# Optimization experiments

Hardware: AMD Instinct MI355X
Metric: run time of the kernel (lower is better)

The kernel has to match this reference:

```python
import jax, jax.numpy as jnp
import numpy as np
from jax import lax

# Module constants (from init_kwargs)
K = 1.0            # conductivity
H = 1.0 / 1023.0   # grid spacing
VALUE = 0.0        # Dirichlet boundary value
STENCIL = np.array([[0.0, 0.25, 0.0],
                    [0.25, 0.0, 0.25],
                    [0.0, 0.25, 0.0]], dtype=np.float32)


def setup_inputs() -> dict:
    key = jax.random.key(0)
    k1, k2 = jax.random.split(key)
    B, C, Hn, Wn = 16, 1, 1024, 1024
    u = jax.random.normal(k1, (B, C, Hn, Wn), dtype=jnp.float32)
    f = jax.random.normal(k2, (B, C, Hn, Wn), dtype=jnp.float32)
    # conv weight: (out=1, in=1, 3, 3), repeated over in_channels (=1 here)
    weight = jnp.asarray(STENCIL).reshape(1, 1, 3, 3)
    return {"u": u, "f": f, "weight": weight}


def reference(u, f, weight):
    # v = detached interior of u, padded with the Dirichlet value
    v_int = lax.stop_gradient(u[..., 1:-1, 1:-1])           # [B,1,H-2,W-2]
    v = jnp.pad(v_int, ((0, 0), (0, 0), (1, 1), (1, 1)),
                mode="constant", constant_values=VALUE)      # [B,1,H,W]
    # 5-point Jacobi stencil, VALID conv -> interior shape [B,1,H-2,W-2]
    conv = lax.conv_general_dilated(
        v, weight, window_strides=(1, 1), padding="VALID",
        dimension_numbers=("NCHW", "OIHW", "NCHW"))
    cof = -(H ** 2) / (K * 4.0)
    source = lax.stop_gradient((cof * f)[..., 1:-1, 1:-1])
    # interior <- stencil(v) + source; boundary stays at Dirichlet VALUE
    out = v.at[..., 1:-1, 1:-1].set(conv + source)
    return out
```

## Files before the change

### kernel.cpp

```cpp
#include <hip/hip_runtime.h>

#define IMG_W 1024
#define IMG_H 1024
#define RPB   4

__global__ __launch_bounds__(256) void dir_rhs_kernel(
    const float* __restrict__ u,
    const float* __restrict__ f,
    const float* __restrict__ wt,
    float* __restrict__ out)
{
    __shared__ float2 halo[RPB + 2][256];

    const int tid = threadIdx.x;
    const int j0  = tid << 2;
    const int gb  = blockIdx.x;
    const int b   = gb >> 8;
    const int r0  = (gb & 255) << 2;
    const size_t img = (size_t)b << 20;

    const float w00 = wt[0], w01 = wt[1], w02 = wt[2];
    const float w10 = wt[3], w11 = wt[4], w12 = wt[5];
    const float w20 = wt[6], w21 = wt[7], w22 = wt[8];
    const float cof = (float)(-(1.0 / 1023.0) * (1.0 / 1023.0) / 4.0);

    float4 stage[RPB + 2];
    #pragma unroll
    for (int k = 0; k < RPB + 2; k++) {
        const int grow = r0 - 1 + k;
        if (grow >= 1 && grow <= IMG_H - 2) {
            stage[k] = *(const float4*)(u + img + (size_t)grow * IMG_W + j0);
        } else {
            stage[k] = make_float4(0.f, 0.f, 0.f, 0.f);
        }
    }
    float4 fr[RPB];
    #pragma unroll
    for (int k = 0; k < RPB; k++) {
        fr[k] = *(const float4*)(f + img + (size_t)(r0 + k) * IMG_W + j0);
    }
    #pragma unroll
    for (int k = 0; k < RPB + 2; k++) {
        if (tid == 0)   stage[k].x = 0.f;
        if (tid == 255) stage[k].w = 0.f;
        halo[k][tid] = make_float2(stage[k].x, stage[k].w);
    }
    __syncthreads();

    const int tl = (tid == 0)   ? 0   : tid - 1;
    const int tr = (tid == 255) ? 255 : tid + 1;

    #pragma unroll
    for (int k = 0; k < RPB; k++) {
        const int grow = r0 + k;
        float4* o4 = (float4*)(out + img + (size_t)grow * IMG_W + j0);
        if (grow == 0 || grow == IMG_H - 1) {
            *o4 = make_float4(0.f, 0.f, 0.f, 0.f);
            continue;
        }
        float vm[6], vc[6], vp[6];
        vm[0] = halo[k    ][tl].y;  vm[5] = halo[k    ][tr].x;
        vc[0] = halo[k + 1][tl].y;  vc[5] = halo[k + 1][tr].x;
        vp[0] = halo[k + 2][tl].y;  vp[5] = halo[k + 2][tr].x;
        vm[1] = stage[k].x;     vm[2] = stage[k].y;     vm[3] = stage[k].z;     vm[4] = stage[k].w;
        vc[1] = stage[k + 1].x; vc[2] = stage[k + 1].y; vc[3] = stage[k + 1].z; vc[4] = stage[k + 1].w;
        vp[1] = stage[k + 2].x; vp[2] = stage[k + 2].y; vp[3] = stage[k + 2].z; vp[4] = stage[k + 2].w;

        const float ff[4] = { fr[k].x, fr[k].y, fr[k].z, fr[k].w };
        float res[4];
        #pragma unroll
        for (int e = 0; e < 4; e++) {
            float acc = cof * ff[e];
            acc += w00 * vm[e] + w01 * vm[e + 1] + w02 * vm[e + 2];
            acc += w10 * vc[e] + w11 * vc[e + 1] + w12 * vc[e + 2];
            acc += w20 * vp[e] + w21 * vp[e + 1] + w22 * vp[e + 2];
            res[e] = acc;
        }
        if (tid == 0)   res[0] = 0.f;
        if (tid == 255) res[3] = 0.f;
        *o4 = make_float4(res[0], res[1], res[2], res[3]);
    }
}

extern "C" void kernel_launch(void* const* d_in, const int* in_sizes, int n_in,
                              void* d_out, int out_size, void* d_ws, size_t ws_size,
                              hipStream_t stream) {
    const float* u  = (const float*)d_in[0];
    const float* f  = (const float*)d_in[1];
    const float* wt = (const float*)d_in[2];
    float* out = (float*)d_out;

    const int B = 16;
    dim3 grid(B * (IMG_H / RPB));
    dim3 block(256);
    dir_rhs_kernel<<<grid, block, 0, stream>>>(u, f, wt, out);
}
```

Before: 171.0 us.

## Use wave-per-row-strip stencil with register rolling, shuffles and nontemporal stores

```diff
diff --git a/kernel.cpp b/kernel.cpp
--- a/kernel.cpp
+++ b/kernel.cpp
@@ -2,7 +2,9 @@
 
 #define IMG_W 1024
 #define IMG_H 1024
-#define RPB   4
+#define RPW   8
+
+typedef float floatx4 __attribute__((ext_vector_type(4)));
 
 __global__ __launch_bounds__(256) void dir_rhs_kernel(
     const float* __restrict__ u,
@@ -10,75 +12,108 @@
     const float* __restrict__ wt,
     float* __restrict__ out)
 {
-    __shared__ float2 halo[RPB + 2][256];
+    const int tid  = threadIdx.x;
+    const int lane = tid & 63;
+    const int wv   = tid >> 6;
+    const int strip = (blockIdx.x << 2) + wv;
+    const int b   = strip >> 7;
+    const int r0  = (strip & 127) * RPW;
+    const int c0  = lane << 4;
+    const size_t img = (size_t)b << 20;
 
-    const int tid = threadIdx.x;
-    const int j0  = tid << 2;
-    const int gb  = blockIdx.x;
-    const int b   = gb >> 8;
-    const int r0  = (gb & 255) << 2;
-    const size_t img = (size_t)b << 20;
+    const float* ub = u + img + c0;
+    const float* fb = f + img + c0;
+    float*       ob = out + img + c0;
 
     const float w00 = wt[0], w01 = wt[1], w02 = wt[2];
     const float w10 = wt[3], w11 = wt[4], w12 = wt[5];
     const float w20 = wt[6], w21 = wt[7], w22 = wt[8];
     const float cof = (float)(-(1.0 / 1023.0) * (1.0 / 1023.0) / 4.0);
 
-    float4 stage[RPB + 2];
-    #pragma unroll
-    for (int k = 0; k < RPB + 2; k++) {
-        const int grow = r0 - 1 + k;
-        if (grow >= 1 && grow <= IMG_H - 2) {
-            stage[k] = *(const float4*)(u + img + (size_t)grow * IMG_W + j0);
+    auto load_v = [&](int g, float* a) {
+        if (g >= 1 && g <= IMG_H - 2) {
+            const floatx4* p = (const floatx4*)(ub + (size_t)g * IMG_W);
+            floatx4 q0 = p[0], q1 = p[1], q2 = p[2], q3 = p[3];
+            a[0]=q0.x; a[1]=q0.y; a[2]=q0.z; a[3]=q0.w;
+            a[4]=q1.x; a[5]=q1.y; a[6]=q1.z; a[7]=q1.w;
+            a[8]=q2.x; a[9]=q2.y; a[10]=q2.z; a[11]=q2.w;
+            a[12]=q3.x; a[13]=q3.y; a[14]=q3.z; a[15]=q3.w;
         } else {
-            stage[k] = make_float4(0.f, 0.f, 0.f, 0.f);
+            #pragma unroll
+            for (int e = 0; e < 16; e++) a[e] = 0.f;
         }
-    }
-    float4 fr[RPB];
-    #pragma unroll
-    for (int k = 0; k < RPB; k++) {
-        fr[k] = *(const float4*)(f + img + (size_t)(r0 + k) * IMG_W + j0);
-    }
-    #pragma unroll
-    for (int k = 0; k < RPB + 2; k++) {
-        if (tid == 0)   stage[k].x = 0.f;
-        if (tid == 255) stage[k].w = 0.f;
-        halo[k][tid] = make_float2(stage[k].x, stage[k].w);
-    }
-    __syncthreads();
+    };
+    auto load_f = [&](int g, float* a) {
+        const floatx4* p = (const floatx4*)(fb + (size_t)g * IMG_W);
+        floatx4 q0 = p[0], q1 = p[1], q2 = p[2], q3 = p[3];
+        a[0]=q0.x; a[1]=q0.y; a[2]=q0.z; a[3]=q0.w;
+        a[4]=q1.x; a[5]=q1.y; a[6]=q1.z; a[7]=q1.w;
+        a[8]=q2.x; a[9]=q2.y; a[10]=q2.z; a[11]=q2.w;
+        a[12]=q3.x; a[13]=q3.y; a[14]=q3.z; a[15]=q3.w;
+    };
+    auto finalize = [&](float* a, float& lh, float& rh) {
+        if (lane == 0)  a[0]  = 0.f;
+        if (lane == 63) a[15] = 0.f;
+        lh = __shfl_up(a[15], 1, 64);
+        rh = __shfl_down(a[0], 1, 64);
+    };
 
-    const int tl = (tid == 0)   ? 0   : tid - 1;
-    const int tr = (tid == 255) ? 255 : tid + 1;
+    float vm[16], vc[16], vp[16], vn[16], fr[16], fn[16];
+    float lhm, rhm, lhc, rhc, lhp, rhp;
+
+    load_v(r0 - 1, vm);
+    load_v(r0,     vc);
+    load_v(r0 + 1, vp);
+    load_f(r0,     fr);
+    finalize(vm, lhm, rhm);
+    finalize(vc, lhc, rhc);
 
     #pragma unroll
-    for (int k = 0; k < RPB; k++) {
-        const int grow = r0 + k;
-        float4* o4 = (float4*)(out + img + (size_t)grow * IMG_W + j0);
-        if (grow == 0 || grow == IMG_H - 1) {
-            *o4 = make_float4(0.f, 0.f, 0.f, 0.f);
-            continue;
+    for (int k = 0; k < RPW; k++) {
+        if (k < RPW - 1) {
+            load_v(r0 + k + 2, vn);
+            load_f(r0 + k + 1, fn);
         }
-        float vm[6], vc[6], vp[6];
-        vm[0] = halo[k    ][tl].y;  vm[5] = halo[k    ][tr].x;
-        vc[0] = halo[k + 1][tl].y;  vc[5] = halo[k + 1][tr].x;
-        vp[0] = halo[k + 2][tl].y;  vp[5] = halo[k + 2][tr].x;
-        vm[1] = stage[k].x;     vm[2] = stage[k].y;     vm[3] = stage[k].z;     vm[4] = stage[k].w;
-        vc[1] = stage[k + 1].x; vc[2] = stage[k + 1].y; vc[3] = stage[k + 1].z; vc[4] = stage[k + 1].w;
-        vp[1] = stage[k + 2].x; vp[2] = stage[k + 2].y; vp[3] = stage[k + 2].z; vp[4] = stage[k + 2].w;
+        finalize(vp, lhp, rhp);
 
-        const float ff[4] = { fr[k].x, fr[k].y, fr[k].z, fr[k].w };
-        float res[4];
+        const int g = r0 + k;
+        float res[16];
         #pragma unroll
-        for (int e = 0; e < 4; e++) {
-            float acc = cof * ff[e];
-            acc += w00 * vm[e] + w01 * vm[e + 1] + w02 * vm[e + 2];
-            acc += w10 * vc[e] + w11 * vc[e + 1] + w12 * vc[e + 2];
-            acc += w20 * vp[e] + w21 * vp[e + 1] + w22 * vp[e + 2];
+        for (int e = 0; e < 16; e++) {
+            const float lm = (e == 0) ? lhm : vm[e - 1];
+            const float rm = (e == 15) ? rhm : vm[e + 1];
+            const float lc = (e == 0) ? lhc : vc[e - 1];
+            const float rc = (e == 15) ? rhc : vc[e + 1];
+            const float lp = (e == 0) ? lhp : vp[e - 1];
+            const float rp = (e == 15) ? rhp : vp[e + 1];
+            float acc = cof * fr[e];
+            acc += w00 * lm + w01 * vm[e] + w02 * rm;
+            acc += w10 * lc + w11 * vc[e] + w12 * rc;
+            acc += w20 * lp + w21 * vp[e] + w22 * rp;
             res[e] = acc;
         }
-        if (tid == 0)   res[0] = 0.f;
-        if (tid == 255) res[3] = 0.f;
-        *o4 = make_float4(res[0], res[1], res[2], res[3]);
+        if (g == 0 || g == IMG_H - 1) {
+            #pragma unroll
+            for (int e = 0; e < 16; e++) res[e] = 0.f;
+        }
+        if (lane == 0)  res[0]  = 0.f;
+        if (lane == 63) res[15] = 0.f;
+
+        floatx4* o4 = (floatx4*)(ob + (size_t)g * IMG_W);
+        floatx4 s0 = { res[0],  res[1],  res[2],  res[3]  };
+        floatx4 s1 = { res[4],  res[5],  res[6],  res[7]  };
+        floatx4 s2 = { res[8],  res[9],  res[10], res[11] };
+        floatx4 s3 = { res[12], res[13], res[14], res[15] };
+        __builtin_nontemporal_store(s0, o4 + 0);
+        __builtin_nontemporal_store(s1, o4 + 1);
+        __builtin_nontemporal_store(s2, o4 + 2);
+        __builtin_nontemporal_store(s3, o4 + 3);
+
+        if (k < RPW - 1) {
+            #pragma unroll
+            for (int e = 0; e < 16; e++) { vm[e] = vc[e]; vc[e] = vp[e]; vp[e] = vn[e]; fr[e] = fn[e]; }
+            lhm = lhc; rhm = rhc; lhc = lhp; rhc = rhp;
+        }
     }
 }
 
@@ -91,7 +126,7 @@
     float* out = (float*)d_out;
 
     const int B = 16;
-    dim3 grid(B * (IMG_H / RPB));
+    dim3 grid(B * (IMG_H / RPW) / 4);
     dim3 block(256);
     dir_rhs_kernel<<<grid, block, 0, stream>>>(u, f, wt, out);
 }
```

Result: slower. 199.5 us (+16.6%).
